# Kernel tuning notes

Hardware: AMD Instinct MI355X
Metric: run time of the kernel (lower is better)

## Reference

```python
import jax, jax.numpy as jnp
import numpy as np

STRIDE = 2

def _conv_transpose3d(x, w_io, stride):
    # x: [N, I, D, H, W]; w_io: [I, O, k2, k3, k4] (torch conv_transpose layout)
    # conv_transpose == lhs-dilated conv with spatially-flipped, IO-swapped kernel
    rhs = jnp.flip(jnp.transpose(w_io, (1, 0, 2, 3, 4)), axis=(2, 3, 4))  # [O, I, k2, k3, k4]
    ks = w_io.shape[2:]
    pad = [(k - 1, k - 1) for k in ks]
    return jax.lax.conv_general_dilated(
        x, rhs, window_strides=(1, 1, 1), padding=pad,
        lhs_dilation=(stride, stride, stride),
        dimension_numbers=('NCDHW', 'OIDHW', 'NCDHW'))


def setup_inputs() -> dict:
    key = jax.random.key(0)
    k1, k2, k3 = jax.random.split(key, 3)
    B, Cin, Cout = 4, 64, 64
    K = (3, 3, 3, 3)
    L = (12, 12, 12, 12)
    init_norm = float(np.sqrt(1.0 / Cout / np.prod(K)))
    x = jax.random.normal(k1, (B, Cin, *L), dtype=jnp.float32)
    weight = init_norm * (2.0 * jax.random.normal(k2, (Cin, Cout, *K), dtype=jnp.float32) - 1.0)
    bias = init_norm * (2.0 * jax.random.normal(k3, (Cout,), dtype=jnp.float32) - 1.0)
    return {'x': x, 'weight': weight, 'bias': bias}


def reference(x, weight, bias):
    # 4D transposed convolution, stride=STRIDE, no padding/dilation, groups=1.
    B, I, L1, L2, L3, L4 = x.shape
    _, O, K1, K2, K3, K4 = weight.shape
    s = STRIDE
    o1 = (L1 - 1) * s + K1
    o2 = (L2 - 1) * s + K2
    o3 = (L3 - 1) * s + K3
    o4 = (L4 - 1) * s + K4
    # Fold first spatial dim into batch; do 3D conv_transpose over the remaining dims.
    xb = jnp.transpose(x, (0, 2, 1, 3, 4, 5)).reshape(B * L1, I, L2, L3, L4)
    out = jnp.zeros((B, O, o1, o2, o3, o4), dtype=x.dtype)
    for ik in range(K1):  # small fixed kernel loop
        y = _conv_transpose3d(xb, weight[:, :, ik], s)           # [B*L1, O, o2, o3, o4]
        y = jnp.transpose(y.reshape(B, L1, O, o2, o3, o4), (0, 2, 1, 3, 4, 5))
        out = out.at[:, :, ik:ik + L1 * s:s].add(y)              # strided scatter-add along dim 1
    out = out + bias[None, :, None, None, None, None]
    return out
```

## Files before the change

### kernel.cpp

```cpp
#include <hip/hip_runtime.h>


typedef short bf16x8 __attribute__((ext_vector_type(8)));
typedef float f32x4 __attribute__((ext_vector_type(4)));

__device__ __forceinline__ unsigned short f2bf(float f) {
    unsigned int u = __float_as_uint(f);
    u = (u + 0x7FFFu + ((u >> 16) & 1u)) >> 16;
    return (unsigned short)u;
}

__global__ __launch_bounds__(256) void wtrans_kernel(const float* __restrict__ w,
                                                     unsigned short* __restrict__ wt) {
    int tid = blockIdx.x * 256 + threadIdx.x;
    if (tid >= 81 * 64 * 64) return;
    int ci = tid & 63;
    int co = (tid >> 6) & 63;
    int kk = tid >> 12;
    wt[tid] = f2bf(w[(ci * 64 + co) * 81 + kk]);
}

#define XS_BYTES 28224
#define WS_BYTES 27648
#define SMEM_BYTES 57344

__global__ __launch_bounds__(512, 2) void convt_mfma_kernel(
        const float* __restrict__ x,
        const unsigned short* __restrict__ wt,
        const float* __restrict__ bias,
        float* __restrict__ out) {

    __shared__ __align__(16) char smem[SMEM_BYTES];
    unsigned short (*xs)[72]     = (unsigned short (*)[72])smem;
    unsigned short (*ws)[64][72] = (unsigned short (*)[64][72])(smem + XS_BYTES);
    float (*stg)[625]            = (float (*)[625])smem;

    int orig = blockIdx.x;
    int xcd = orig & 7, oj = orig >> 3;
    int wg = (xcd < 4 ? xcd * 313 : 1252 + (xcd - 4) * 312) + oj;
    int p2 = wg % 25; int tq = wg / 25;
    int p1 = tq % 25; int b = tq / 25;

    int i1v[2], k1v[2], n1 = 0;
    { int h = p1 >> 1, q = p1 & 1;
      for (int s = 0; s < 2 - q; ++s) { int i = h - s; if (0 <= i && i < 12) { i1v[n1] = i; k1v[n1] = 2 * s + q; ++n1; } } }
    int i2v[2], k2v[2], n2 = 0;
    { int h = p2 >> 1, q = p2 & 1;
      for (int s = 0; s < 2 - q; ++s) { int i = h - s; if (0 <= i && i < 12) { i2v[n2] = i; k2v[n2] = 2 * s + q; ++n2; } } }
    int ncomb = n1 * n2;

    int tid = threadIdx.x;
    int lane = tid & 63, wave = tid >> 6;
    int n_lo = lane & 15, quad = lane >> 4;

    int cls = wave >> 1, hw = wave & 1;
    int r3 = cls >> 1, r4 = cls & 1;
    int n4 = 13 - r4;
    int N = (13 - r3) * n4;
    int ntiles = (N + 15) >> 4;
    int nt4 = 2 - r4;

    int nmyt = 0; int pe3a[6], pe4a[6], posa[6];
    #pragma unroll
    for (int j = 0; j < 6; ++j) {
        int t = hw + 2 * j;
        if (t < ntiles) {
            int pos = t * 16 + n_lo;
            int cp = pos < N ? pos : N - 1;
            pe3a[j] = cp / n4; pe4a[j] = cp - pe3a[j] * n4; posa[j] = pos;
            nmyt = j + 1;
        }
    }

    for (int f = tid; f < XS_BYTES / 4; f += 512) ((int*)smem)[f] = 0;

    f32x4 acc[6][4];
    #pragma unroll
    for (int mt = 0; mt < 4; ++mt) {
        #pragma unroll
        for (int rg = 0; rg < 4; ++rg) {
            float bv = bias[mt * 16 + quad * 4 + rg];
            #pragma unroll
            for (int j = 0; j < 6; ++j) acc[j][mt][rg] = bv;
        }
    }
    __syncthreads();

    for (int c = 0; c < ncomb; ++c) {
        if (c) __syncthreads();
        int c1 = c / n2, c2 = c - (c / n2) * n2;
        int i1 = i1v[c1], k1 = k1v[c1];
        int i2 = i2v[c2], k2 = k2v[c2];

        const float* xb = x + (size_t)b * 64 * 20736 + i1 * 1728 + i2 * 144;
        for (int it = 0; it < 5; ++it) {
            int f = it * 512 + tid;
            if (f < 2304) {
                int ci = f / 36, cc = f - 36 * ci;
                float4 v = *(const float4*)(xb + (size_t)ci * 20736 + cc * 4);
                #pragma unroll
                for (int u = 0; u < 4; ++u) {
                    int e = cc * 4 + u;
                    int a3 = e / 12, a4 = e - a3 * 12;
                    xs[(a3 + 1) * 14 + (a4 + 1)][ci] = f2bf(((const float*)&v)[u]);
                }
            }
        }

        int kb9 = (k1 * 3 + k2) * 9;
        for (int g = 0; g < 3; ++g) {
            if (g) __syncthreads();
            const bf16x8* wsrc = (const bf16x8*)(wt + (size_t)(kb9 + 3 * g) * 4096);
            #pragma unroll
            for (int it = 0; it < 3; ++it) {
                int idx = it * 512 + tid;
                int tp = idx >> 9, rch = idx & 511;
                *(bf16x8*)&ws[tp][rch >> 3][(rch & 7) << 3] = wsrc[idx];
            }
            __syncthreads();

            if ((g & 1) == r3) {
                int s3 = (g - r3) >> 1;
                for (int s4 = 0; s4 < nt4; ++s4) {
                    int k4 = 2 * s4 + r4;
                    #pragma unroll
                    for (int kc = 0; kc < 2; ++kc) {
                        int kof = kc * 32 + quad * 8;
                        bf16x8 a0  = *(const bf16x8*)&ws[k4][n_lo     ][kof];
                        bf16x8 a1  = *(const bf16x8*)&ws[k4][n_lo + 16][kof];
                        bf16x8 a2  = *(const bf16x8*)&ws[k4][n_lo + 32][kof];
                        bf16x8 a3v = *(const bf16x8*)&ws[k4][n_lo + 48][kof];
                        #pragma unroll
                        for (int j = 0; j < 6; ++j) {
                            if (j < nmyt) {
                                int row = (pe3a[j] - s3 + 1) * 14 + (pe4a[j] - s4 + 1);
                                bf16x8 bb = *(const bf16x8*)&xs[row][kof];
                                acc[j][0] = __builtin_amdgcn_mfma_f32_16x16x32_bf16(a0,  bb, acc[j][0], 0, 0, 0);
                                acc[j][1] = __builtin_amdgcn_mfma_f32_16x16x32_bf16(a1,  bb, acc[j][1], 0, 0, 0);
                                acc[j][2] = __builtin_amdgcn_mfma_f32_16x16x32_bf16(a2,  bb, acc[j][2], 0, 0, 0);
                                acc[j][3] = __builtin_amdgcn_mfma_f32_16x16x32_bf16(a3v, bb, acc[j][3], 0, 0, 0);
                            }
                        }
                    }
                }
            }
        }
    }

    __syncthreads();

    size_t obase = (size_t)b * 64 * 390625 + (size_t)(p1 * 25 + p2) * 625;
    #pragma unroll
    for (int ch = 0; ch < 4; ++ch) {
        #pragma unroll
        for (int j = 0; j < 6; ++j) {
            if (j < nmyt && posa[j] < N) {
                int p34 = (2 * pe3a[j] + r3) * 25 + (2 * pe4a[j] + r4);
                #pragma unroll
                for (int rg = 0; rg < 4; ++rg)
                    stg[quad * 4 + rg][p34] = acc[j][ch][rg];
            }
        }
        __syncthreads();
        for (int idx = tid; idx < 10000; idx += 512) {
            int co_l = idx / 625, e = idx - 625 * co_l;
            out[obase + (size_t)(ch * 16 + co_l) * 390625 + e] = stg[co_l][e];
        }
        __syncthreads();
    }
}

extern "C" void kernel_launch(void* const* d_in, const int* in_sizes, int n_in,
                              void* d_out, int out_size, void* d_ws, size_t ws_size,
                              hipStream_t stream) {
    const float* x    = (const float*)d_in[0];
    const float* w    = (const float*)d_in[1];
    const float* bias = (const float*)d_in[2];
    float* out = (float*)d_out;
    unsigned short* wt = (unsigned short*)d_ws;

    wtrans_kernel<<<(81 * 64 * 64 + 255) / 256, 256, 0, stream>>>(w, wt);
    convt_mfma_kernel<<<2500, 512, 0, stream>>>(x, wt, bias, out);
}
```

Measured before the change: 616.9 us.

## Pre-transpose input to bf16, swizzle LDS, and rebalance output tiles across waves

```diff
diff --git a/kernel.cpp b/kernel.cpp
--- a/kernel.cpp
+++ b/kernel.cpp
@@ -20,20 +20,42 @@
     wt[tid] = f2bf(w[(ci * 64 + co) * 81 + kk]);
 }
 
-#define XS_BYTES 28224
-#define WS_BYTES 27648
-#define SMEM_BYTES 57344
-
-__global__ __launch_bounds__(512, 2) void convt_mfma_kernel(
-        const float* __restrict__ x,
+__global__ __launch_bounds__(256) void xtrans_kernel(const float* __restrict__ x,
+                                                     unsigned short* __restrict__ xb) {
+    __shared__ unsigned short ls[144][72];
+    int blk = blockIdx.x;
+    int i2 = blk % 12; int t = blk / 12; int i1 = t % 12; int b = t / 12;
+    int tid = threadIdx.x;
+    int ci = tid >> 2, sub = tid & 3;
+    const float* src = x + (size_t)b * 1327104 + (size_t)ci * 20736 + i1 * 1728 + i2 * 144 + sub * 36;
+    #pragma unroll
+    for (int q = 0; q < 9; ++q) {
+        float4 v = *(const float4*)(src + q * 4);
+        #pragma unroll
+        for (int u = 0; u < 4; ++u) ls[sub * 36 + q * 4 + u][ci] = f2bf(((const float*)&v)[u]);
+    }
+    __syncthreads();
+    unsigned short* dst = xb + (size_t)blk * 9216;
+    for (int c = tid; c < 1152; c += 256) {
+        int m = c >> 3, part = c & 7;
+        *(bf16x8*)(dst + c * 8) = *(const bf16x8*)((const char*)ls + m * 144 + part * 16);
+    }
+}
+
+#define XS_BYTES 25088
+#define WS_BYTES 24576
+#define SMEM_BYTES 49664
+
+__global__ __launch_bounds__(512, 4) void convt_mfma_kernel(
+        const unsigned short* __restrict__ xb,
         const unsigned short* __restrict__ wt,
         const float* __restrict__ bias,
         float* __restrict__ out) {
 
     __shared__ __align__(16) char smem[SMEM_BYTES];
-    unsigned short (*xs)[72]     = (unsigned short (*)[72])smem;
-    unsigned short (*ws)[64][72] = (unsigned short (*)[64][72])(smem + XS_BYTES);
-    float (*stg)[625]            = (float (*)[625])smem;
+    char* xsb = smem;
+    char* wsb = smem + XS_BYTES;
+    float (*stg)[625] = (float (*)[625])smem;
 
     int orig = blockIdx.x;
     int xcd = orig & 7, oj = orig >> 3;
@@ -50,29 +72,37 @@
     int ncomb = n1 * n2;
 
     int tid = threadIdx.x;
-    int lane = tid & 63, wave = tid >> 6;
+    int lane = tid & 63;
+    int wave = __builtin_amdgcn_readfirstlane(tid >> 6);
     int n_lo = lane & 15, quad = lane >> 4;
 
-    int cls = wave >> 1, hw = wave & 1;
-    int r3 = cls >> 1, r4 = cls & 1;
-    int n4 = 13 - r4;
-    int N = (13 - r3) * n4;
-    int ntiles = (N + 15) >> 4;
-    int nt4 = 2 - r4;
-
-    int nmyt = 0; int pe3a[6], pe4a[6], posa[6];
+    static const int NSLOT[8] = {4, 4, 5, 5, 5, 5, 6, 6};
+    static const signed char SCLS[8][6] = {
+        {0,0,2,2,0,0}, {0,0,2,2,0,0}, {0,0,3,3,3,0}, {0,0,3,3,3,0},
+        {0,0,3,3,3,0}, {0,1,1,2,2,0}, {1,1,1,1,2,2}, {1,1,1,1,2,2}};
+    static const signed char STILE[8][6] = {
+        {0,1,0,1,0,0}, {2,3,2,3,0,0}, {4,5,0,1,2,0}, {6,7,3,4,5,0},
+        {8,9,6,7,8,0}, {10,0,1,4,5,0}, {2,3,4,5,6,7}, {6,7,8,9,8,9}};
+
+    int ns = NSLOT[wave];
+    int use0 = 0, use1 = 0, use2 = 0, use3 = 0;
+    int rbase[6]; unsigned vis = 0;
     #pragma unroll
     for (int j = 0; j < 6; ++j) {
-        int t = hw + 2 * j;
-        if (t < ntiles) {
-            int pos = t * 16 + n_lo;
-            int cp = pos < N ? pos : N - 1;
-            pe3a[j] = cp / n4; pe4a[j] = cp - pe3a[j] * n4; posa[j] = pos;
-            nmyt = j + 1;
-        }
-    }
-
-    for (int f = tid; f < XS_BYTES / 4; f += 512) ((int*)smem)[f] = 0;
+        int c = SCLS[wave][j], t = STILE[wave][j];
+        int r3 = c >> 1, r4 = c & 1;
+        int n4 = 13 - r4, N = (13 - r3) * n4;
+        int pos = t * 16 + n_lo;
+        int cp = pos < N ? pos : N - 1;
+        int pe3 = cp / n4, pe4 = cp - pe3 * n4;
+        rbase[j] = (pe3 + 1) * 14 + (pe4 + 1);
+        if (j < ns) {
+            if (pos < N) vis |= 1u << j;
+            use0 |= (c == 0); use1 |= (c == 1); use2 |= (c == 2); use3 |= (c == 3);
+        }
+    }
+
+    for (int f = tid; f < XS_BYTES / 4; f += 512) ((int*)xsb)[f] = 0;
 
     f32x4 acc[6][4];
     #pragma unroll
@@ -92,54 +122,59 @@
         int i1 = i1v[c1], k1 = k1v[c1];
         int i2 = i2v[c2], k2 = k2v[c2];
 
-        const float* xb = x + (size_t)b * 64 * 20736 + i1 * 1728 + i2 * 144;
-        for (int it = 0; it < 5; ++it) {
-            int f = it * 512 + tid;
-            if (f < 2304) {
-                int ci = f / 36, cc = f - 36 * ci;
-                float4 v = *(const float4*)(xb + (size_t)ci * 20736 + cc * 4);
-                #pragma unroll
-                for (int u = 0; u < 4; ++u) {
-                    int e = cc * 4 + u;
-                    int a3 = e / 12, a4 = e - a3 * 12;
-                    xs[(a3 + 1) * 14 + (a4 + 1)][ci] = f2bf(((const float*)&v)[u]);
-                }
+        const unsigned short* xbs = xb + (size_t)((b * 12 + i1) * 12 + i2) * 9216;
+        #pragma unroll
+        for (int it = 0; it < 3; ++it) {
+            int idx = it * 512 + tid;
+            if (idx < 1152) {
+                bf16x8 v = *(const bf16x8*)(xbs + idx * 8);
+                int m = idx >> 3, part = idx & 7;
+                int a3 = (m * 2731) >> 15, a4 = m - a3 * 12;
+                int r = (a3 + 1) * 14 + a4 + 1;
+                *(bf16x8*)(xsb + r * 128 + ((part ^ (r & 7)) << 4)) = v;
             }
         }
 
         int kb9 = (k1 * 3 + k2) * 9;
         for (int g = 0; g < 3; ++g) {
             if (g) __syncthreads();
-            const bf16x8* wsrc = (const bf16x8*)(wt + (size_t)(kb9 + 3 * g) * 4096);
+            const unsigned short* wsrc = wt + (size_t)(kb9 + 3 * g) * 4096;
             #pragma unroll
             for (int it = 0; it < 3; ++it) {
                 int idx = it * 512 + tid;
-                int tp = idx >> 9, rch = idx & 511;
-                *(bf16x8*)&ws[tp][rch >> 3][(rch & 7) << 3] = wsrc[idx];
+                bf16x8 v = *(const bf16x8*)(wsrc + idx * 8);
+                int tap = idx >> 9, rch = idx & 511;
+                int co = rch >> 3, part = rch & 7;
+                *(bf16x8*)(wsb + tap * 8192 + co * 128 + ((part ^ (co & 7)) << 4)) = v;
             }
             __syncthreads();
 
-            if ((g & 1) == r3) {
-                int s3 = (g - r3) >> 1;
-                for (int s4 = 0; s4 < nt4; ++s4) {
-                    int k4 = 2 * s4 + r4;
+            int p = g & 1, s3 = (g - p) >> 1;
+            #pragma unroll
+            for (int tap = 0; tap < 3; ++tap) {
+                const int par = tap & 1;
+                int any = par ? (p ? use3 : use1) : (p ? use2 : use0);
+                if (!any) continue;
+                int s4 = tap >> 1;
+                const char* wst = wsb + tap * 8192;
+                int need = 2 * p + par;
+                #pragma unroll
+                for (int kc = 0; kc < 2; ++kc) {
+                    int pr = kc * 4 + quad;
+                    int pwa = (pr ^ (n_lo & 7)) << 4;
+                    bf16x8 a0  = *(const bf16x8*)(wst + n_lo * 128 + pwa);
+                    bf16x8 a1  = *(const bf16x8*)(wst + n_lo * 128 + 2048 + pwa);
+                    bf16x8 a2  = *(const bf16x8*)(wst + n_lo * 128 + 4096 + pwa);
+                    bf16x8 a3v = *(const bf16x8*)(wst + n_lo * 128 + 6144 + pwa);
                     #pragma unroll
-                    for (int kc = 0; kc < 2; ++kc) {
-                        int kof = kc * 32 + quad * 8;
-                        bf16x8 a0  = *(const bf16x8*)&ws[k4][n_lo     ][kof];
-                        bf16x8 a1  = *(const bf16x8*)&ws[k4][n_lo + 16][kof];
-                        bf16x8 a2  = *(const bf16x8*)&ws[k4][n_lo + 32][kof];
-                        bf16x8 a3v = *(const bf16x8*)&ws[k4][n_lo + 48][kof];
-                        #pragma unroll
-                        for (int j = 0; j < 6; ++j) {
-                            if (j < nmyt) {
-                                int row = (pe3a[j] - s3 + 1) * 14 + (pe4a[j] - s4 + 1);
-                                bf16x8 bb = *(const bf16x8*)&xs[row][kof];
-                                acc[j][0] = __builtin_amdgcn_mfma_f32_16x16x32_bf16(a0,  bb, acc[j][0], 0, 0, 0);
-                                acc[j][1] = __builtin_amdgcn_mfma_f32_16x16x32_bf16(a1,  bb, acc[j][1], 0, 0, 0);
-                                acc[j][2] = __builtin_amdgcn_mfma_f32_16x16x32_bf16(a2,  bb, acc[j][2], 0, 0, 0);
-                                acc[j][3] = __builtin_amdgcn_mfma_f32_16x16x32_bf16(a3v, bb, acc[j][3], 0, 0, 0);
-                            }
+                    for (int j = 0; j < 6; ++j) {
+                        if (j < ns && SCLS[wave][j] == need) {
+                            int row = rbase[j] - s3 * 14 - s4;
+                            bf16x8 bb = *(const bf16x8*)(xsb + row * 128 + ((pr ^ (row & 7)) << 4));
+                            acc[j][0] = __builtin_amdgcn_mfma_f32_16x16x32_bf16(a0,  bb, acc[j][0], 0, 0, 0);
+                            acc[j][1] = __builtin_amdgcn_mfma_f32_16x16x32_bf16(a1,  bb, acc[j][1], 0, 0, 0);
+                            acc[j][2] = __builtin_amdgcn_mfma_f32_16x16x32_bf16(a2,  bb, acc[j][2], 0, 0, 0);
+                            acc[j][3] = __builtin_amdgcn_mfma_f32_16x16x32_bf16(a3v, bb, acc[j][3], 0, 0, 0);
                         }
                     }
                 }
@@ -154,16 +189,21 @@
     for (int ch = 0; ch < 4; ++ch) {
         #pragma unroll
         for (int j = 0; j < 6; ++j) {
-            if (j < nmyt && posa[j] < N) {
-                int p34 = (2 * pe3a[j] + r3) * 25 + (2 * pe4a[j] + r4);
+            if ((vis >> j) & 1) {
+                int cc = SCLS[wave][j];
+                int r3 = cc >> 1, r4 = cc & 1;
+                int rb = rbase[j] - 15;
+                int pe3 = (rb * 2341) >> 15;
+                int pe4 = rb - 14 * pe3;
+                int p34 = (2 * pe3 + r3) * 25 + 2 * pe4 + r4;
                 #pragma unroll
                 for (int rg = 0; rg < 4; ++rg)
                     stg[quad * 4 + rg][p34] = acc[j][ch][rg];
             }
         }
         __syncthreads();
-        for (int idx = tid; idx < 10000; idx += 512) {
-            int co_l = idx / 625, e = idx - 625 * co_l;
+        for (int idx2 = tid; idx2 < 10000; idx2 += 512) {
+            int co_l = idx2 / 625, e = idx2 - 625 * co_l;
             out[obase + (size_t)(ch * 16 + co_l) * 390625 + e] = stg[co_l][e];
         }
         __syncthreads();
@@ -178,7 +218,9 @@
     const float* bias = (const float*)d_in[2];
     float* out = (float*)d_out;
     unsigned short* wt = (unsigned short*)d_ws;
+    unsigned short* xbf = wt + 81 * 64 * 64;
 
     wtrans_kernel<<<(81 * 64 * 64 + 255) / 256, 256, 0, stream>>>(w, wt);
-    convt_mfma_kernel<<<2500, 512, 0, stream>>>(x, wt, bias, out);
-}
+    xtrans_kernel<<<576, 256, 0, stream>>>(x, xbf);
+    convt_mfma_kernel<<<2500, 512, 0, stream>>>(xbf, wt, bias, out);
+}
```

Result: slower. 652.2 us (+5.7%).
